# Performance work log

Measured on AMD Instinct MI355X. Metric: run time of the kernel, lower is better.

Reference implementation:

```python
import jax, jax.numpy as jnp
import numpy as np

N_NODES = 512
EMB = 64
TIME_LAG = 8
TIME_LOG = 5.0
EPS = 1e-6
LN_EPS = 1e-5


def _linear(x, w, b):
    return x @ w.T + b


def _lrelu(x):
    return jax.nn.leaky_relu(x, 0.01)


def _layer_norm(x, g, b):
    m = x.mean(-1, keepdims=True)
    v = jnp.var(x, axis=-1, keepdims=True)
    return (x - m) * jax.lax.rsqrt(v + LN_EPS) * g + b


def _forward(skill_seq, time_seq, label_seq, adj, node_embeddings,
             msg_fc1_w, msg_fc1_b, msg_fc2_w, msg_fc2_b,
             f_w1, f_b1, f_ln1_g, f_ln1_b, f_w2, f_b2, f_ln2_g, f_ln2_b, f_w3, f_b3):
    bs, T = skill_seq.shape
    L = TIME_LAG
    steps = T - L
    N, E = N_NODES, EMB

    # emb_history == 0 label remap: 0 -> -1, -1 -> 0, 1 -> 1
    lp = jnp.where(label_seq == 0, -2, label_seq)
    lp = jnp.where(lp == -1, 0, lp)
    lp = jnp.where(lp == -2, -1, lp)

    tf = time_seq.astype(jnp.float32)
    delta_t = jnp.log(jnp.abs(tf[:, :, None] - tf[:, None, :]) + EPS) / jnp.log(TIME_LOG)  # [bs,T,T]

    # initial hidden: scatter last-occurrence embedding of each skill in warmup window
    s0 = skill_seq[:, :L]
    emb_init = node_embeddings[s0] * lp[:, :L, None].astype(jnp.float32)  # [bs,L,E]
    eq = s0[:, :, None] == s0[:, None, :]
    later = jnp.triu(jnp.ones((L, L), bool), 1)
    is_last = ~jnp.any(eq & later, axis=2)  # [bs,L] True at last occurrence
    hidden0 = jnp.zeros((bs, N, E), jnp.float32).at[jnp.arange(bs)[:, None], s0].add(
        emb_init * is_last[..., None])

    # spatial adjacency stack [adj, adj^2/N], batch-major [bs,K,2,N,N]
    adj2 = jnp.matmul(adj, adj) / N
    asp = jnp.transpose(jnp.stack([adj, adj2], axis=2), (1, 0, 2, 3, 4))

    win = jnp.arange(steps)[:, None] + jnp.arange(L)[None, :]  # [steps,L], entry = t-L+i
    sh_all = skill_seq[:, win]                                  # [bs,steps,L]
    tgt_all = skill_seq[:, L:]                                  # [bs,steps]
    b3 = jnp.arange(bs)[:, None, None]
    # delta_t.transpose(-1,-2)[:, t, t-L:t] == delta_t[:, t-L:t, t]
    dtw_all = delta_t[b3, win[None], (jnp.arange(steps) + L)[None, :, None]]  # [bs,steps,L]

    b_col = jnp.arange(bs)[:, None]
    b_row = jnp.arange(bs)

    def step(hidden, x):
        sh, dtw, tgt = x  # [bs,L], [bs,L], [bs]
        hh = hidden[b_col, sh]  # [bs,L,E]
        # cross_weight = adj_spatial[:, arange(bs), :, skill_history] -> [bs,K,2,L,N]
        cw = jnp.take_along_axis(asp, sh[:, None, None, :, None], axis=3)
        pre = jnp.concatenate([
            jnp.broadcast_to(hh[:, :, None, :], (bs, L, N, E)),
            jnp.broadcast_to(hidden[:, None, :, :], (bs, L, N, E)),
        ], axis=-1)  # [bs,L,N,2E]
        msg = jnp.tanh(_linear(pre, msg_fc1_w, msg_fc1_b))
        msg = jnp.tanh(_linear(msg, msg_fc2_w, msg_fc2_b))  # [bs,L,N,E]
        msg = msg * jnp.exp(-dtw)[:, :, None, None]          # fold time decay into msg
        # sum over spatial hop s and lag l without materializing [bs,K,2,L,N,E]
        agg = jnp.einsum('bksln,blne->bkne', cw, msg)        # [bs,K,N,E]
        new_hidden = agg.mean(axis=1)
        # final MLP (causica-style generate_fully_connected):
        # res(Linear+LReLU), res(LN+Linear+LReLU), LN, Linear -> 2
        h = agg + _lrelu(_linear(agg, f_w1, f_b1))
        h = h + _lrelu(_linear(_layer_norm(h, f_ln1_g, f_ln1_b), f_w2, f_b2))
        logits = _linear(_layer_norm(h, f_ln2_g, f_ln2_b), f_w3, f_b3)  # [bs,K,N,2]
        p = jax.nn.softmax(logits, axis=-1)
        pred = p[b_row, :, tgt, 1:]  # [bs,K,1]
        return new_hidden, pred

    xs = (jnp.transpose(sh_all, (1, 0, 2)), jnp.transpose(dtw_all, (1, 0, 2)), tgt_all.T)
    _, preds = jax.lax.scan(step, hidden0, xs)
    return preds  # [steps, bs, K, 1]


def setup_inputs() -> dict:
    key = jax.random.key(0)
    ks = jax.random.split(key, 12)
    bs, T, N, E, K = 16, 20, N_NODES, EMB, 2
    return {
        'skill_seq': jax.random.randint(ks[0], (bs, T), 0, N),
        'time_seq': jnp.sort(jax.random.randint(ks[1], (bs, T), 0, 100000), axis=-1),
        'label_seq': jax.random.randint(ks[2], (bs, T), 0, 2),
        'adj': jax.random.uniform(ks[3], (K, bs, N, N), jnp.float32),
        'node_embeddings': jax.random.normal(ks[4], (N, E), jnp.float32),
        'msg_fc1_w': jax.random.normal(ks[5], (E, 2 * E), jnp.float32) / np.sqrt(2 * E).astype(np.float32),
        'msg_fc1_b': jnp.zeros((E,), jnp.float32),
        'msg_fc2_w': jax.random.normal(ks[6], (E, E), jnp.float32) / np.sqrt(E).astype(np.float32),
        'msg_fc2_b': jnp.zeros((E,), jnp.float32),
        'f_w1': jax.random.normal(ks[7], (E, E), jnp.float32) / np.sqrt(E).astype(np.float32),
        'f_b1': jnp.zeros((E,), jnp.float32),
        'f_ln1_g': jnp.ones((E,), jnp.float32),
        'f_ln1_b': jnp.zeros((E,), jnp.float32),
        'f_w2': jax.random.normal(ks[8], (E, E), jnp.float32) / np.sqrt(E).astype(np.float32),
        'f_b2': jnp.zeros((E,), jnp.float32),
        'f_ln2_g': jnp.ones((E,), jnp.float32),
        'f_ln2_b': jnp.zeros((E,), jnp.float32),
        'f_w3': jax.random.normal(ks[9], (2, E), jnp.float32) / np.sqrt(E).astype(np.float32),
        'f_b3': jnp.zeros((2,), jnp.float32),
    }


def reference(skill_seq, time_seq, label_seq, adj, node_embeddings,
              msg_fc1_w, msg_fc1_b, msg_fc2_w, msg_fc2_b,
              f_w1, f_b1, f_ln1_g, f_ln1_b, f_w2, f_b2, f_ln2_g, f_ln2_b, f_w3, f_b3):
    return _forward(skill_seq, time_seq, label_seq, adj, node_embeddings,
                    msg_fc1_w, msg_fc1_b, msg_fc2_w, msg_fc2_b,
                    f_w1, f_b1, f_ln1_g, f_ln1_b, f_w2, f_b2, f_ln2_g, f_ln2_b, f_w3, f_b3)
```

## Files before the change

### kernel.cpp

```cpp
#include <hip/hip_runtime.h>
#include <hip/hip_bf16.h>

#define BS 16
#define TT 20
#define STEPS 12
#define NN 512
#define EE 64

typedef __attribute__((ext_vector_type(8))) short bfrag8;
typedef __attribute__((ext_vector_type(4))) float f32x4;
typedef unsigned short ushort_t;
typedef unsigned int uint_t;

#define MFMA16(a,b,c) __builtin_amdgcn_mfma_f32_16x16x32_bf16(a,b,c,0,0,0)

#if __has_builtin(__builtin_amdgcn_rcpf)
#define RCP(x) __builtin_amdgcn_rcpf(x)
#else
#define RCP(x) (1.0f/(x))
#endif

__device__ __forceinline__ float tanh_fast(float x) {
  float t = __expf(-2.f * fabsf(x));
  float r = (1.f - t) * RCP(1.f + t);
  return copysignf(r, x);
}

__device__ __forceinline__ float lrelu(float x) { return x > 0.f ? x : 0.01f * x; }

__device__ __forceinline__ float wsum64(float x) {
  #pragma unroll
  for (int off = 32; off > 0; off >>= 1) x += __shfl_xor(x, off);
  return x;
}

__device__ __forceinline__ ushort_t f2bf(float f) {
  uint_t u = __float_as_uint(f);
  u += 0x7fffu + ((u >> 16) & 1u);
  return (ushort_t)(u >> 16);
}

__global__ __launch_bounds__(256) void setup_kernel(
    const int* __restrict__ skill, const float* __restrict__ adj,
    float* __restrict__ crow)
{
  __shared__ __align__(16) float a_rows[19*516];
  __shared__ __align__(16) float a_cols[5*516];
  __shared__ float red[95*2];
  __shared__ int s_node[5];

  int tid = threadIdx.x, bid = blockIdx.x;
  int kb = bid >> 2, pq = bid & 3;
  int b = kb & 15;
  const float* A = adj + (size_t)kb*NN*NN;

  for (int idx = tid; idx < 19*512; idx += 256) {
    int tpos = idx >> 9, m = idx & 511;
    a_rows[tpos*516 + m] = A[(size_t)skill[b*TT + tpos]*NN + m];
  }
  if (tid < 5) s_node[tid] = skill[b*TT + pq*5 + tid];
  __syncthreads();
  for (int idx = tid; idx < 5*512; idx += 256) {
    int p = idx >> 9, m = idx & 511;
    a_cols[p*516 + m] = A[(size_t)m*NN + s_node[p]];
  }
  __syncthreads();

  int pr = tid & 127, mh = tid >> 7;
  if (pr < 95) {
    int tpos = pr / 5, p = pr % 5;
    const float4* ra = (const float4*)&a_rows[tpos*516 + mh*256];
    const float4* rc = (const float4*)&a_cols[p*516 + mh*256];
    float s = 0.f;
    #pragma unroll 8
    for (int i = 0; i < 64; ++i) {
      float4 x = ra[i], y = rc[i];
      s += x.x*y.x + x.y*y.y + x.z*y.z + x.w*y.w;
    }
    red[pr*2 + mh] = s;
  }
  __syncthreads();
  if (tid < 95) {
    int tpos = tid / 5, p = tid % 5;
    float dot = red[tid*2] + red[tid*2 + 1];
    crow[(size_t)kb*380 + tpos*20 + pq*5 + p] =
        a_rows[tpos*516 + s_node[p]] + dot * (1.f/512.f);
  }
}

__global__ __launch_bounds__(512) void step_kernel(
    const int* __restrict__ skill, const int* __restrict__ timeq,
    const int* __restrict__ label, const float* __restrict__ nemb,
    const float* __restrict__ W1, const float* __restrict__ W2,
    const float* __restrict__ b1, const float* __restrict__ b2,
    const float* __restrict__ crow, float* __restrict__ agg_tgt)
{
  __shared__ __align__(16) ushort_t sWa[64*72];
  __shared__ __align__(16) ushort_t sWb[64*72];
  __shared__ __align__(16) ushort_t sW2[64*72];
  __shared__ __align__(16) ushort_t sH[32*72];
  __shared__ __align__(16) float sTV[20*72];
  __shared__ __align__(16) float sTU[8*72];
  __shared__ __align__(16) ushort_t sM1[160*72];
  __shared__ float sCROW[2*19*20];
  __shared__ float sED[STEPS*8];
  __shared__ int sSK[TT];

  int tid = threadIdx.x, b = blockIdx.x;
  int w = tid >> 6, lane = tid & 63, q = lane >> 4, nn = lane & 15;
  int ct = w & 3, half = w >> 2, epos = ct*16 + nn;

  if (tid < TT) sSK[tid] = skill[b*TT + tid];
  for (int idx = tid; idx < 4096; idx += 512) {
    int e = idx >> 6, j = idx & 63;
    sWa[e*72 + j] = f2bf(W1[e*128 + j]);
    sWb[e*72 + j] = f2bf(W1[e*128 + 64 + j]);
    sW2[e*72 + j] = f2bf(W2[e*64 + j]);
  }
  for (int idx = tid; idx < 760; idx += 512) {
    int k = idx / 380, r2 = idx % 380;
    sCROW[idx] = crow[(size_t)(k*BS + b)*380 + r2];
  }
  if (tid < STEPS*8) {
    int s = tid >> 3, l = tid & 7;
    float d = fabsf((float)(timeq[b*TT + s + l] - timeq[b*TT + s + 8]));
    sED[tid] = expf(-logf(d + 1e-6f) * 0.6213349345596119f);
  }
  __syncthreads();

  for (int idx = tid; idx < 32*64; idx += 512) {
    int p = idx >> 6, e = idx & 63;
    ushort_t hv = 0;
    if (p < 20) {
      int node = sSK[p];
      int lstar = -1;
      #pragma unroll
      for (int l = 0; l < 8; ++l) if (sSK[l] == node) lstar = l;
      if (lstar >= 0) {
        float lp = (label[b*TT + lstar] == 1) ? 1.f : -1.f;
        hv = f2bf(nemb[node*EE + e] * lp);
      }
    }
    sH[p*72 + e] = hv;
  }
  __syncthreads();

  bfrag8 wb0 = *(const bfrag8*)&sWb[epos*72 + q*8];
  bfrag8 wb1 = *(const bfrag8*)&sWb[epos*72 + 32 + q*8];
  bfrag8 wa0 = *(const bfrag8*)&sWa[epos*72 + q*8];
  bfrag8 wa1 = *(const bfrag8*)&sWa[epos*72 + 32 + q*8];
  bfrag8 w20 = *(const bfrag8*)&sW2[epos*72 + q*8];
  bfrag8 w21 = *(const bfrag8*)&sW2[epos*72 + 32 + q*8];
  float b1v = b1[epos], b2v = b2[epos];

  for (int t = 0; t < STEPS; ++t) {
    if (half == 0) {
      bfrag8 a0 = *(const bfrag8*)&sH[nn*72 + q*8];
      bfrag8 a1 = *(const bfrag8*)&sH[nn*72 + 32 + q*8];
      f32x4 accV = {0,0,0,0};
      accV = MFMA16(a0, wb0, accV);
      accV = MFMA16(a1, wb1, accV);
      int ur = (nn < 8) ? (t + nn) : 24;
      bfrag8 u0 = *(const bfrag8*)&sH[ur*72 + q*8];
      bfrag8 u1 = *(const bfrag8*)&sH[ur*72 + 32 + q*8];
      f32x4 accU = {0,0,0,0};
      accU = MFMA16(u0, wa0, accU);
      accU = MFMA16(u1, wa1, accU);
      #pragma unroll
      for (int r = 0; r < 4; ++r)
        sTV[(q*4 + r)*72 + epos] = tanh_fast(accV[r]);
      if (q < 2) {
        #pragma unroll
        for (int r = 0; r < 4; ++r)
          sTU[(q*4 + r)*72 + epos] = tanh_fast(accU[r] + b1v);
      }
    } else {
      bfrag8 a0 = *(const bfrag8*)&sH[(16 + nn)*72 + q*8];
      bfrag8 a1 = *(const bfrag8*)&sH[(16 + nn)*72 + 32 + q*8];
      f32x4 accV = {0,0,0,0};
      accV = MFMA16(a0, wb0, accV);
      accV = MFMA16(a1, wb1, accV);
      if (q == 0) {
        #pragma unroll
        for (int r = 0; r < 4; ++r)
          sTV[(16 + r)*72 + epos] = tanh_fast(accV[r]);
      }
    }
    __syncthreads();

    {
      int pp = tid >> 5, ep = tid & 31;
      for (int p = pp; p < 20; p += 16) {
        float2 tv2 = *(const float2*)&sTV[p*72 + 2*ep];
        #pragma unroll
        for (int l = 0; l < 8; ++l) {
          float2 tu2 = *(const float2*)&sTU[l*72 + 2*ep];
          float2 num, den, m;
          num.x = tu2.x + tv2.x;            num.y = tu2.y + tv2.y;
          den.x = fmaf(tu2.x, tv2.x, 1.f);  den.y = fmaf(tu2.y, tv2.y, 1.f);
          den.x = fmaxf(den.x, 1e-30f);     den.y = fmaxf(den.y, 1e-30f);
          m.x = num.x * RCP(den.x);         m.y = num.y * RCP(den.y);
          __hip_bfloat162 h2 = __float22bfloat162_rn(m);
          *(__hip_bfloat162*)&sM1[(p*8 + l)*72 + 2*ep] = h2;
        }
      }
    }
    __syncthreads();

    const float* edt = &sED[t*8];
    #pragma unroll
    for (int rr = 0; rr < 5; ++rr) {
      int rt = half*5 + rr;
      bfrag8 a0 = *(const bfrag8*)&sM1[(rt*16 + nn)*72 + q*8];
      bfrag8 a1 = *(const bfrag8*)&sM1[(rt*16 + nn)*72 + 32 + q*8];
      f32x4 z = {0,0,0,0};
      z = MFMA16(a0, w20, z);
      z = MFMA16(a1, w21, z);
      int p = rt*2 + (q >> 1);
      float ag0 = 0.f, ag1 = 0.f;
      #pragma unroll
      for (int r = 0; r < 4; ++r) {
        int l = (q & 1)*4 + r;
        float m2 = tanh_fast(z[r] + b2v) * edt[l];
        ag0 = fmaf(sCROW[(t + l)*20 + p], m2, ag0);
        ag1 = fmaf(sCROW[380 + (t + l)*20 + p], m2, ag1);
      }
      ag0 += __shfl_xor(ag0, 16);
      ag1 += __shfl_xor(ag1, 16);
      if ((q & 1) == 0) {
        sH[p*72 + epos] = f2bf(0.5f*(ag0 + ag1));
        if (p == t + 8) {
          agg_tgt[((t*BS + b)*2 + 0)*EE + epos] = ag0;
          agg_tgt[((t*BS + b)*2 + 1)*EE + epos] = ag1;
        }
      }
    }
    __syncthreads();
  }
}

__global__ __launch_bounds__(64) void pred_kernel(
    const float* __restrict__ agg_tgt,
    const float* __restrict__ fw1, const float* __restrict__ fb1,
    const float* __restrict__ g1, const float* __restrict__ be1,
    const float* __restrict__ fw2, const float* __restrict__ fb2,
    const float* __restrict__ g2, const float* __restrict__ be2,
    const float* __restrict__ fw3, const float* __restrict__ fb3,
    float* __restrict__ out)
{
  int ts = blockIdx.x >> 4, b = blockIdx.x & 15;
  int e = threadIdx.x;
  __shared__ float sx[64];
  for (int k = 0; k < 2; ++k) {
    float x = agg_tgt[((ts*BS + b)*2 + k)*EE + e];
    sx[e] = x;
    __syncthreads();
    float y = fb1[e];
    for (int j = 0; j < 64; ++j) y = fmaf(sx[j], fw1[e*64 + j], y);
    float h1 = x + lrelu(y);
    float mean1 = wsum64(h1) * (1.f/64.f);
    float d1 = h1 - mean1;
    float var1 = wsum64(d1*d1) * (1.f/64.f);
    float xn = d1 * rsqrtf(var1 + 1e-5f) * g1[e] + be1[e];
    __syncthreads();
    sx[e] = xn;
    __syncthreads();
    float z = fb2[e];
    for (int j = 0; j < 64; ++j) z = fmaf(sx[j], fw2[e*64 + j], z);
    float h2 = h1 + lrelu(z);
    float mean2 = wsum64(h2) * (1.f/64.f);
    float d2 = h2 - mean2;
    float var2 = wsum64(d2*d2) * (1.f/64.f);
    float xn2 = d2 * rsqrtf(var2 + 1e-5f) * g2[e] + be2[e];
    float p0 = wsum64(xn2 * fw3[e]);
    float p1 = wsum64(xn2 * fw3[64 + e]);
    if (e == 0) {
      float l0 = p0 + fb3[0], l1 = p1 + fb3[1];
      out[(ts*BS + b)*2 + k] = 1.f / (1.f + expf(l0 - l1));
    }
    __syncthreads();
  }
}

extern "C" void kernel_launch(void* const* d_in, const int* in_sizes, int n_in,
                              void* d_out, int out_size, void* d_ws, size_t ws_size,
                              hipStream_t stream) {
  const int*   skill = (const int*)d_in[0];
  const int*   timeq = (const int*)d_in[1];
  const int*   label = (const int*)d_in[2];
  const float* adj   = (const float*)d_in[3];
  const float* nemb  = (const float*)d_in[4];
  const float* W1    = (const float*)d_in[5];
  const float* b1    = (const float*)d_in[6];
  const float* W2    = (const float*)d_in[7];
  const float* b2    = (const float*)d_in[8];
  float* out = (float*)d_out;

  float* crow    = (float*)d_ws;
  float* agg_tgt = crow + 32*380;

  setup_kernel<<<128, 256, 0, stream>>>(skill, adj, crow);
  step_kernel<<<16, 512, 0, stream>>>(skill, timeq, label, nemb, W1, W2,
                                      b1, b2, crow, agg_tgt);
  pred_kernel<<<STEPS*BS, 64, 0, stream>>>(agg_tgt,
      (const float*)d_in[9],  (const float*)d_in[10],
      (const float*)d_in[11], (const float*)d_in[12],
      (const float*)d_in[13], (const float*)d_in[14],
      (const float*)d_in[15], (const float*)d_in[16],
      (const float*)d_in[17], (const float*)d_in[18], out);
}
```

Baseline: 165.2 us.

## Fuse prediction MLP into step kernel, keeping aggregates in shared memory

Removes the separate pred_kernel launch by running the two-layer MLP, layer norms and output head at the end of step_kernel. The target aggregates stay in shared memory instead of going through a global workspace. The fw1/fw2 weights are staged into LDS, reusing the sM1 buffer, and sTV/sTU are merged into one buffer so sFP can hold the normalized intermediates. The prediction work now runs on only 16 blocks instead of 192 small ones, trading lower parallelism for one fewer launch and one fewer global round trip.

New measurement: 164.4 us. Within noise of the previous version (-0.5%).

```diff
diff --git a/kernel.cpp b/kernel.cpp
--- a/kernel.cpp
+++ b/kernel.cpp
@@ -93,17 +93,23 @@
     const int* __restrict__ label, const float* __restrict__ nemb,
     const float* __restrict__ W1, const float* __restrict__ W2,
     const float* __restrict__ b1, const float* __restrict__ b2,
-    const float* __restrict__ crow, float* __restrict__ agg_tgt)
+    const float* __restrict__ crow,
+    const float* __restrict__ fw1, const float* __restrict__ fb1,
+    const float* __restrict__ g1, const float* __restrict__ be1,
+    const float* __restrict__ fw2, const float* __restrict__ fb2,
+    const float* __restrict__ g2, const float* __restrict__ be2,
+    const float* __restrict__ fw3, const float* __restrict__ fb3,
+    float* __restrict__ out)
 {
   __shared__ __align__(16) ushort_t sWa[64*72];
   __shared__ __align__(16) ushort_t sWb[64*72];
   __shared__ __align__(16) ushort_t sW2[64*72];
   __shared__ __align__(16) ushort_t sH[32*72];
-  __shared__ __align__(16) float sTV[20*72];
-  __shared__ __align__(16) float sTU[8*72];
+  __shared__ __align__(16) float sFP[28*72];
   __shared__ __align__(16) ushort_t sM1[160*72];
   __shared__ float sCROW[2*19*20];
   __shared__ float sED[STEPS*8];
+  __shared__ float sAGG[24*68];
   __shared__ int sSK[TT];
 
   int tid = threadIdx.x, b = blockIdx.x;
@@ -168,11 +174,11 @@
       accU = MFMA16(u1, wa1, accU);
       #pragma unroll
       for (int r = 0; r < 4; ++r)
-        sTV[(q*4 + r)*72 + epos] = tanh_fast(accV[r]);
+        sFP[(q*4 + r)*72 + epos] = tanh_fast(accV[r]);
       if (q < 2) {
         #pragma unroll
         for (int r = 0; r < 4; ++r)
-          sTU[(q*4 + r)*72 + epos] = tanh_fast(accU[r] + b1v);
+          sFP[(20 + q*4 + r)*72 + epos] = tanh_fast(accU[r] + b1v);
       }
     } else {
       bfrag8 a0 = *(const bfrag8*)&sH[(16 + nn)*72 + q*8];
@@ -183,7 +189,7 @@
       if (q == 0) {
         #pragma unroll
         for (int r = 0; r < 4; ++r)
-          sTV[(16 + r)*72 + epos] = tanh_fast(accV[r]);
+          sFP[(16 + r)*72 + epos] = tanh_fast(accV[r]);
       }
     }
     __syncthreads();
@@ -191,10 +197,10 @@
     {
       int pp = tid >> 5, ep = tid & 31;
       for (int p = pp; p < 20; p += 16) {
-        float2 tv2 = *(const float2*)&sTV[p*72 + 2*ep];
+        float2 tv2 = *(const float2*)&sFP[p*72 + 2*ep];
         #pragma unroll
         for (int l = 0; l < 8; ++l) {
-          float2 tu2 = *(const float2*)&sTU[l*72 + 2*ep];
+          float2 tu2 = *(const float2*)&sFP[(20 + l)*72 + 2*ep];
           float2 num, den, m;
           num.x = tu2.x + tv2.x;            num.y = tu2.y + tv2.y;
           den.x = fmaf(tu2.x, tv2.x, 1.f);  den.y = fmaf(tu2.y, tv2.y, 1.f);
@@ -230,55 +236,66 @@
       if ((q & 1) == 0) {
         sH[p*72 + epos] = f2bf(0.5f*(ag0 + ag1));
         if (p == t + 8) {
-          agg_tgt[((t*BS + b)*2 + 0)*EE + epos] = ag0;
-          agg_tgt[((t*BS + b)*2 + 1)*EE + epos] = ag1;
+          sAGG[(t*2 + 0)*68 + epos] = ag0;
+          sAGG[(t*2 + 1)*68 + epos] = ag1;
         }
       }
     }
     __syncthreads();
   }
-}
-
-__global__ __launch_bounds__(64) void pred_kernel(
-    const float* __restrict__ agg_tgt,
-    const float* __restrict__ fw1, const float* __restrict__ fb1,
-    const float* __restrict__ g1, const float* __restrict__ be1,
-    const float* __restrict__ fw2, const float* __restrict__ fb2,
-    const float* __restrict__ g2, const float* __restrict__ be2,
-    const float* __restrict__ fw3, const float* __restrict__ fb3,
-    float* __restrict__ out)
-{
-  int ts = blockIdx.x >> 4, b = blockIdx.x & 15;
-  int e = threadIdx.x;
-  __shared__ float sx[64];
-  for (int k = 0; k < 2; ++k) {
-    float x = agg_tgt[((ts*BS + b)*2 + k)*EE + e];
-    sx[e] = x;
-    __syncthreads();
-    float y = fb1[e];
-    for (int j = 0; j < 64; ++j) y = fmaf(sx[j], fw1[e*64 + j], y);
+
+  float* fwLDS = (float*)sM1;
+  float* sXN   = sFP;
+
+  for (int idx = tid; idx < 4096; idx += 512)
+    fwLDS[(idx >> 6)*65 + (idx & 63)] = fw1[idx];
+  __syncthreads();
+
+  int e = lane;
+  float h1s[3];
+  float fb1v = fb1[e], g1v = g1[e], be1v = be1[e];
+  #pragma unroll
+  for (int r3 = 0; r3 < 3; ++r3) {
+    int task = r3*8 + w;
+    const float* xv = &sAGG[task*68];
+    float x = xv[e];
+    float y = fb1v;
+    for (int j = 0; j < 64; ++j) y = fmaf(xv[j], fwLDS[e*65 + j], y);
     float h1 = x + lrelu(y);
     float mean1 = wsum64(h1) * (1.f/64.f);
     float d1 = h1 - mean1;
     float var1 = wsum64(d1*d1) * (1.f/64.f);
-    float xn = d1 * rsqrtf(var1 + 1e-5f) * g1[e] + be1[e];
-    __syncthreads();
-    sx[e] = xn;
-    __syncthreads();
-    float z = fb2[e];
-    for (int j = 0; j < 64; ++j) z = fmaf(sx[j], fw2[e*64 + j], z);
-    float h2 = h1 + lrelu(z);
+    float xn = d1 * rsqrtf(var1 + 1e-5f) * g1v + be1v;
+    sXN[task*68 + e] = xn;
+    h1s[r3] = h1;
+  }
+  __syncthreads();
+
+  for (int idx = tid; idx < 4096; idx += 512)
+    fwLDS[(idx >> 6)*65 + (idx & 63)] = fw2[idx];
+  __syncthreads();
+
+  float fb2v = fb2[e], g2v = g2[e], be2v = be2[e];
+  float w3a = fw3[e], w3b = fw3[64 + e];
+  float fb30 = fb3[0], fb31 = fb3[1];
+  #pragma unroll
+  for (int r3 = 0; r3 < 3; ++r3) {
+    int task = r3*8 + w;
+    const float* xnv = &sXN[task*68];
+    float z = fb2v;
+    for (int j = 0; j < 64; ++j) z = fmaf(xnv[j], fwLDS[e*65 + j], z);
+    float h2 = h1s[r3] + lrelu(z);
     float mean2 = wsum64(h2) * (1.f/64.f);
     float d2 = h2 - mean2;
     float var2 = wsum64(d2*d2) * (1.f/64.f);
-    float xn2 = d2 * rsqrtf(var2 + 1e-5f) * g2[e] + be2[e];
-    float p0 = wsum64(xn2 * fw3[e]);
-    float p1 = wsum64(xn2 * fw3[64 + e]);
+    float xn2 = d2 * rsqrtf(var2 + 1e-5f) * g2v + be2v;
+    float p0 = wsum64(xn2 * w3a);
+    float p1 = wsum64(xn2 * w3b);
     if (e == 0) {
-      float l0 = p0 + fb3[0], l1 = p1 + fb3[1];
-      out[(ts*BS + b)*2 + k] = 1.f / (1.f + expf(l0 - l1));
-    }
-    __syncthreads();
+      int ts = task >> 1, kk = task & 1;
+      float l0 = p0 + fb30, l1 = p1 + fb31;
+      out[(ts*BS + b)*2 + kk] = 1.f / (1.f + expf(l0 - l1));
+    }
   }
 }
 
@@ -296,13 +313,11 @@
   const float* b2    = (const float*)d_in[8];
   float* out = (float*)d_out;
 
-  float* crow    = (float*)d_ws;
-  float* agg_tgt = crow + 32*380;
+  float* crow = (float*)d_ws;
 
   setup_kernel<<<128, 256, 0, stream>>>(skill, adj, crow);
   step_kernel<<<16, 512, 0, stream>>>(skill, timeq, label, nemb, W1, W2,
-                                      b1, b2, crow, agg_tgt);
-  pred_kernel<<<STEPS*BS, 64, 0, stream>>>(agg_tgt,
+      b1, b2, crow,
       (const float*)d_in[9],  (const float*)d_in[10],
       (const float*)d_in[11], (const float*)d_in[12],
       (const float*)d_in[13], (const float*)d_in[14],
```
